# Performance work log

Measured on AMD Instinct MI355X. Metric: run time of the kernel, lower is better.

The kernel has to match this reference:

```python
import jax, jax.numpy as jnp
from jax import lax
import numpy as np

GWS = (2, 7, 7)          # grid_window_size
NUM_HEADS = 4
DIM = 256
HEAD_DIM = DIM // NUM_HEADS
SCALE = HEAD_DIM ** -0.5


def _rel_index(ws):
    d, h, w = ws
    coords = np.stack(np.meshgrid(np.arange(d), np.arange(h), np.arange(w), indexing='ij')).reshape(3, -1)
    rel = (coords[:, :, None] - coords[:, None, :]).transpose(1, 2, 0)
    rel[:, :, 0] += d - 1
    rel[:, :, 1] += h - 1
    rel[:, :, 2] += w - 1
    rel[:, :, 0] *= (2 * h - 1) * (2 * w - 1)
    rel[:, :, 1] *= (2 * w - 1)
    return rel.sum(-1)

RPI = jnp.asarray(_rel_index(GWS))  # (98, 98) int, constant buffer


def _ln(x, w, b, eps=1e-5):
    m = x.mean(-1, keepdims=True)
    v = ((x - m) ** 2).mean(-1, keepdims=True)
    return (x - m) * lax.rsqrt(v + eps) * w + b


def _attention(x, qkv_w, proj_w, proj_b, bias_table):
    # x: (num_windows, N, C); qkv has no bias in the original (qkv_bias=False)
    Bw, N, C = x.shape
    qkv = (x @ qkv_w.T).reshape(Bw, N, 3, NUM_HEADS, HEAD_DIM).transpose(2, 0, 3, 1, 4)
    q, k, v = qkv[0] * SCALE, qkv[1], qkv[2]
    scores = jnp.einsum('bhnd,bhmd->bhnm', q, k)
    bias = bias_table[RPI.reshape(-1)].reshape(N, N, NUM_HEADS).transpose(2, 0, 1)
    a = jax.nn.softmax(scores + bias[None], axis=-1)
    out = jnp.einsum('bhnm,bhmd->bhnd', a, v).transpose(0, 2, 1, 3).reshape(Bw, N, C)
    return out @ proj_w.T + proj_b


def _window_partition(x):
    B, D, H, W, C = x.shape
    d, h, w = GWS
    x = x.reshape(B, D // d, d, H // h, h, W // w, w, C).transpose(0, 1, 3, 5, 2, 4, 6, 7)
    return x.reshape(-1, d * h * w, C)


def _window_reverse(win, B, D, H, W):
    d, h, w = GWS
    x = win.reshape(B, D // d, H // h, W // w, d, h, w, -1).transpose(0, 1, 4, 2, 5, 3, 6, 7)
    return x.reshape(B, D, H, W, -1)


def _grid_partition(x):
    B, D, H, W, C = x.shape
    d, h, w = GWS
    x = x.reshape(B, d, D // d, h, H // h, w, W // w, C).transpose(0, 2, 4, 6, 1, 3, 5, 7)
    return x.reshape(-1, d * h * w, C)


def _grid_reverse(g, B, D, H, W):
    d, h, w = GWS
    x = g.reshape(B, D // d, H // h, W // w, d, h, w, -1).transpose(0, 4, 1, 5, 2, 6, 3, 7)
    return x.reshape(B, D, H, W, -1)


def _conv3d(x, w, b):
    y = lax.conv_general_dilated(x, w, (1, 1, 1), 'SAME',
                                 dimension_numbers=('NCDHW', 'OIDHW', 'NCDHW'))
    return y + b[None, :, None, None, None]


def _leaky(x):
    return jnp.where(x >= 0, x, 0.01 * x)


def setup_inputs() -> dict:
    key = jax.random.key(0)
    ks = jax.random.split(key, 12)
    B, D, H, W = 2, 8, 56, 56
    dim = DIM
    TBL = (2 * GWS[0] - 1) * (2 * GWS[1] - 1) * (2 * GWS[2] - 1)  # 507
    p = lambda k, s: jax.random.normal(k, s, jnp.float32) * 0.02
    return {
        'input': jax.random.normal(ks[0], (B, dim, D, H, W), jnp.float32),
        'n1w': jnp.ones((dim,), jnp.float32), 'n1b': jnp.zeros((dim,), jnp.float32),
        'n2w': jnp.ones((dim,), jnp.float32), 'n2b': jnp.zeros((dim,), jnp.float32),
        'wqkv': p(ks[1], (3 * dim, dim)),
        'wprojw': p(ks[2], (dim, dim)), 'wprojb': jnp.zeros((dim,), jnp.float32),
        'wbias': p(ks[3], (TBL, NUM_HEADS)),
        'gqkv': p(ks[4], (3 * dim, dim)),
        'gprojw': p(ks[5], (dim, dim)), 'gprojb': jnp.zeros((dim,), jnp.float32),
        'gbias': p(ks[6], (TBL, NUM_HEADS)),
        'f1c1w': p(ks[7], (128, 128, 3, 3, 3)), 'f1c1b': jnp.zeros((128,), jnp.float32),
        'f1c2w': p(ks[8], (128, 128, 3, 3, 3)), 'f1c2b': jnp.zeros((128,), jnp.float32),
        'g1c1w': p(ks[9], (128, 128, 3, 3, 3)), 'g1c1b': jnp.zeros((128,), jnp.float32),
        'g1c2w': p(ks[10], (128, 128, 3, 3, 3)), 'g1c2b': jnp.zeros((128,), jnp.float32),
    }


def reference(input, n1w, n1b, n2w, n2b, wqkv, wprojw, wprojb, wbias,
              gqkv, gprojw, gprojb, gbias,
              f1c1w, f1c1b, f1c2w, f1c2b, g1c1w, g1c1b, g1c2w, g1c2b):
    B, C, D, H, W = input.shape
    x = input.transpose(0, 2, 3, 4, 1)  # b d h w c
    x = _ln(x, n1w, n1b)
    pd = (GWS[0] - D % GWS[0]) % GWS[0]
    ph = (GWS[1] - H % GWS[1]) % GWS[1]
    pw = (GWS[2] - W % GWS[2]) % GWS[2]
    if pd or ph or pw:
        x = jnp.pad(x, ((0, 0), (0, pd), (0, ph), (0, pw), (0, 0)))
    Dp, Hp, Wp = D + pd, H + ph, W + pw
    # block (window) attention
    win = _window_partition(x)
    win = _attention(win, wqkv, wprojw, wprojb, wbias)
    xw = _window_reverse(win, B, Dp, Hp, Wp)
    # grid attention
    y = _ln(xw, n2w, n2b)
    g = _grid_partition(y)
    g = _attention(g, gqkv, gprojw, gprojb, gbias)
    y = _grid_reverse(g, B, Dp, Hp, Wp) + xw
    if pd or ph or pw:
        y = y[:, :D, :H, :W, :]
    y = y.transpose(0, 4, 1, 2, 3)  # b c d h w
    s = input + y
    # reversible conv block: split 256 -> 128/128
    x1, x2 = s[:, :C // 2], s[:, C // 2:]
    y1 = x1 + _conv3d(_leaky(_conv3d(x2, f1c1w, f1c1b)), f1c2w, f1c2b)
    y2 = x2 + _conv3d(_leaky(_conv3d(y1, g1c1w, g1c1b)), g1c2w, g1c2b)
    return jnp.concatenate([y1, y2], axis=1)
```

## Files before the change

### kernel.cpp

```cpp
#include <hip/hip_runtime.h>
#include <stdint.h>


typedef unsigned short u16;
typedef __attribute__((ext_vector_type(8))) short short8;
typedef __attribute__((ext_vector_type(4))) float f32x4;

#define TOK   50176
#define CH    256
#define SPAT  25088
#define PLANE 3136

__device__ __forceinline__ float b2f(u16 u) {
    union { uint32_t i; float f; } v; v.i = ((uint32_t)u) << 16; return v.f;
}
__device__ __forceinline__ u16 f2b(float f) {
    union { float f; uint32_t i; } v; v.f = f;
    uint32_t i = v.i;
    uint32_t r = i + 0x7FFFu + ((i >> 16) & 1u);
    return (u16)(r >> 16);
}

__global__ __launch_bounds__(256) void cvtw_kernel(
    const float* __restrict__ src, u16* __restrict__ dst)
{
    int i = (blockIdx.x * 256 + threadIdx.x) * 4;
    float4 v = *(const float4*)(src + i);
    ushort4 p;
    p.x = f2b(v.x); p.y = f2b(v.y); p.z = f2b(v.z); p.w = f2b(v.w);
    *(ushort4*)(dst + i) = p;
}

__global__ __launch_bounds__(256) void ln1_kernel(
    const float* __restrict__ x, const float* __restrict__ w,
    const float* __restrict__ bsh, u16* __restrict__ out)
{
    int t = blockIdx.x * 256 + threadIdx.x;
    int b = t / SPAT, sp = t % SPAT;
    const float* px = x + (size_t)b * CH * SPAT + sp;
    float s = 0.f, ss = 0.f;
    for (int c = 0; c < CH; c++) { float v = px[(size_t)c * SPAT]; s += v; ss += v * v; }
    float mean = s * (1.0f / CH);
    float var  = ss * (1.0f / CH) - mean * mean;
    float rstd = rsqrtf(var + 1e-5f);
    u16* po = out + (size_t)t * CH;
    for (int c = 0; c < CH; c++) {
        float v = (px[(size_t)c * SPAT] - mean) * rstd * w[c] + bsh[c];
        po[c] = f2b(v);
    }
}

__global__ __launch_bounds__(256) void ln2_kernel(
    const u16* __restrict__ x, const float* __restrict__ w,
    const float* __restrict__ bsh, u16* __restrict__ out)
{
    int wave = threadIdx.x >> 6, lane = threadIdx.x & 63;
    int t = blockIdx.x * 4 + wave;
    const u16* px = x + (size_t)t * CH + lane * 4;
    ushort4 v4 = *(const ushort4*)px;
    float v0 = b2f(v4.x), v1 = b2f(v4.y), v2 = b2f(v4.z), v3 = b2f(v4.w);
    float s = v0 + v1 + v2 + v3;
    float ss = v0*v0 + v1*v1 + v2*v2 + v3*v3;
    for (int o = 32; o > 0; o >>= 1) {
        s  += __shfl_xor(s,  o, 64);
        ss += __shfl_xor(ss, o, 64);
    }
    float mean = s * (1.0f / CH);
    float rstd = rsqrtf(ss * (1.0f / CH) - mean * mean + 1e-5f);
    float4 w4 = *(const float4*)(w + lane * 4);
    float4 b4 = *(const float4*)(bsh + lane * 4);
    ushort4 o4;
    o4.x = f2b((v0 - mean) * rstd * w4.x + b4.x);
    o4.y = f2b((v1 - mean) * rstd * w4.y + b4.y);
    o4.z = f2b((v2 - mean) * rstd * w4.z + b4.z);
    o4.w = f2b((v3 - mean) * rstd * w4.w + b4.w);
    *(ushort4*)(out + (size_t)t * CH + lane * 4) = o4;
}

__global__ __launch_bounds__(256) void gemm_mfma_kernel(
    const u16* __restrict__ A, const u16* __restrict__ B,
    const float* __restrict__ bias, const u16* __restrict__ res,
    u16* __restrict__ C, int Nout)
{
    __shared__ u16 sAg[128][72];
    __shared__ u16 sBg[128][72];
    int tid = threadIdx.x;
    int m0 = blockIdx.x * 128, n0g = blockIdx.y * 128;
    int lane = tid & 63, wv = tid >> 6;
    int quad = lane >> 4, l15 = lane & 15;
    int mw = (wv & 1) * 64, nw = (wv >> 1) * 64;

    f32x4 zz = {0.f, 0.f, 0.f, 0.f};
    f32x4 acc[4][4];
    #pragma unroll
    for (int i = 0; i < 4; i++)
        #pragma unroll
        for (int j = 0; j < 4; j++) acc[i][j] = zz;

    for (int kc = 0; kc < 256; kc += 64) {
        __syncthreads();
        #pragma unroll
        for (int i = 0; i < 4; i++) {
            int unit = tid + i * 256;
            int row = unit >> 3, k8 = (unit & 7) << 3;
            *(uint4*)&sAg[row][k8] = *(const uint4*)(A + (size_t)(m0 + row) * 256 + kc + k8);
        }
        #pragma unroll
        for (int i = 0; i < 4; i++) {
            int unit = tid + i * 256;
            int row = unit >> 3, k8 = (unit & 7) << 3;
            *(uint4*)&sBg[row][k8] = *(const uint4*)(B + (size_t)(n0g + row) * 256 + kc + k8);
        }
        __syncthreads();
        #pragma unroll
        for (int kk = 0; kk < 2; kk++) {
            short8 afr[4], bfr[4];
            #pragma unroll
            for (int mt = 0; mt < 4; mt++)
                afr[mt] = *(const short8*)&sAg[mw + mt*16 + l15][kk*32 + quad*8];
            #pragma unroll
            for (int nt = 0; nt < 4; nt++)
                bfr[nt] = *(const short8*)&sBg[nw + nt*16 + l15][kk*32 + quad*8];
            #pragma unroll
            for (int mt = 0; mt < 4; mt++)
                #pragma unroll
                for (int nt = 0; nt < 4; nt++)
                    acc[mt][nt] = __builtin_amdgcn_mfma_f32_16x16x32_bf16(
                        afr[mt], bfr[nt], acc[mt][nt], 0, 0, 0);
        }
    }

    #pragma unroll
    for (int nt = 0; nt < 4; nt++) {
        int n = n0g + nw + nt*16 + l15;
        float bv = bias ? bias[n] : 0.f;
        #pragma unroll
        for (int mt = 0; mt < 4; mt++) {
            int m = m0 + mw + mt*16 + quad*4;
            #pragma unroll
            for (int r = 0; r < 4; r++) {
                float v = acc[mt][nt][r] + bv;
                size_t off = (size_t)(m + r) * Nout + n;
                if (res) v += b2f(res[off]);
                C[off] = f2b(v);
            }
        }
    }
}

__global__ __launch_bounds__(256) void attn_mfma_kernel(
    const u16* __restrict__ qkv, const float* __restrict__ btab,
    u16* __restrict__ outp, int mode)
{
    __shared__ u16 sKV[8704];
    __shared__ u16 sS[112][136];
    __shared__ float sBias[507];
    __shared__ int sTok[112];
    __shared__ int sEnc[112];
    __shared__ float sInv[112];

    int g = blockIdx.x, head = blockIdx.y, tid = threadIdx.x;
    int b  = g >> 8;
    int gd = (g >> 6) & 3, gh = (g >> 3) & 7, gw = g & 7;

    int lane = tid & 63, wv = tid >> 6;
    int quad = lane >> 4, l15 = lane & 15;
    int mts[2] = {wv, wv + 4};

    if (tid < 112) {
        int t = tid;
        int i = t / 49, r = t % 49, j = r / 7, k = r % 7;
        sEnc[tid] = i * 169 + j * 13 + k;
        int tokv = 0;
        if (t < 98) {
            int d, h, w;
            if (mode == 0) { d = gd*2 + i; h = gh*7 + j; w = gw*7 + k; }
            else           { d = i*4 + gd; h = j*8 + gh; w = k*8 + gw; }
            tokv = ((b*8 + d)*56 + h)*56 + w;
        }
        sTok[tid] = tokv;
    }
    for (int idx = tid; idx < 507; idx += 256) sBias[idx] = btab[idx * 4 + head];
    __syncthreads();

    for (int idx = tid; idx < 112 * 8; idx += 256) {
        int row = idx >> 3, c8 = (idx & 7) << 3;
        uint4 v = {0u, 0u, 0u, 0u};
        if (row < 98)
            v = *(const uint4*)(qkv + (size_t)sTok[row] * 768 + 256 + head * 64 + c8);
        *(uint4*)&sKV[row * 72 + c8] = v;
    }
    __syncthreads();

    short8 qf[2][2];
    #pragma unroll
    for (int mi = 0; mi < 2; mi++) {
        int mt = mts[mi];
        #pragma unroll
        for (int ks = 0; ks < 2; ks++) {
            short8 v;
            #pragma unroll
            for (int j = 0; j < 8; j++) v[j] = 0;
            int row = mt * 16 + l15;
            if (mt < 7 && row < 98)
                v = *(const short8*)(qkv + (size_t)sTok[row] * 768 + head * 64 + ks * 32 + quad * 8);
            qf[mi][ks] = v;
        }
    }

    f32x4 zz = {0.f, 0.f, 0.f, 0.f};
    #pragma unroll
    for (int mi = 0; mi < 2; mi++) {
        int mt = mts[mi];
        if (mt >= 7) continue;
        for (int nt = 0; nt < 7; nt++) {
            f32x4 acc = zz;
            acc = __builtin_amdgcn_mfma_f32_16x16x32_bf16(
                qf[mi][0], *(const short8*)&sKV[(nt*16 + l15) * 72 + quad*8], acc, 0, 0, 0);
            acc = __builtin_amdgcn_mfma_f32_16x16x32_bf16(
                qf[mi][1], *(const short8*)&sKV[(nt*16 + l15) * 72 + 32 + quad*8], acc, 0, 0, 0);
            int n = nt * 16 + l15;
            int en = (n < 98) ? sEnc[n] : 0;
            #pragma unroll
            for (int r = 0; r < 4; r++) {
                int m = mt * 16 + quad * 4 + r;
                float v;
                if (n < 98) {
                    int em = sEnc[m < 98 ? m : 97];
                    v = acc[r] * 0.125f + sBias[em - en + 253];
                } else v = -1e30f;
                sS[m][n] = f2b(v);
            }
        }
    }
    __syncthreads();

    for (int idx = tid; idx < 64 * 30; idx += 256) {
        int c = idx / 30, t = 98 + idx % 30;
        sKV[c * 136 + t] = 0;
    }
    for (int idx = tid; idx < 98 * 8; idx += 256) {
        int tok = idx >> 3, c8 = (idx & 7) << 3;
        uint4 v = *(const uint4*)(qkv + (size_t)sTok[tok] * 768 + 512 + head * 64 + c8);
        const u16* pv = (const u16*)&v;
        #pragma unroll
        for (int j = 0; j < 8; j++) sKV[(c8 + j) * 136 + tok] = pv[j];
    }

    {
        int row = tid >> 1, half = tid & 1;
        if (row < 112) {
            #pragma unroll
            for (int j = 0; j < 8; j++) sS[row][112 + half * 8 + j] = 0;
        }
        if (row < 98) {
            int c0 = half * 49;
            float mx = -1e30f;
            for (int j = 0; j < 49; j++) mx = fmaxf(mx, b2f(sS[row][c0 + j]));
            mx = fmaxf(mx, __shfl_xor(mx, 1, 64));
            float sum = 0.f;
            for (int j = 0; j < 49; j++) {
                float e = __expf(b2f(sS[row][c0 + j]) - mx);
                sum += e;
                sS[row][c0 + j] = f2b(e);
            }
            sum += __shfl_xor(sum, 1, 64);
            if (half == 0) sInv[row] = 1.0f / sum;
        }
    }
    __syncthreads();

    f32x4 po[2][4];
    #pragma unroll
    for (int mi = 0; mi < 2; mi++)
        #pragma unroll
        for (int nt = 0; nt < 4; nt++) po[mi][nt] = zz;

    #pragma unroll
    for (int mi = 0; mi < 2; mi++) {
        int mt = mts[mi];
        if (mt >= 7) continue;
        for (int ks = 0; ks < 4; ks++) {
            short8 ap = *(const short8*)&sS[mt*16 + l15][ks*32 + quad*8];
            #pragma unroll
            for (int nt = 0; nt < 4; nt++) {
                short8 bv = *(const short8*)&sKV[(nt*16 + l15) * 136 + ks*32 + quad*8];
                po[mi][nt] = __builtin_amdgcn_mfma_f32_16x16x32_bf16(ap, bv, po[mi][nt], 0, 0, 0);
            }
        }
    }

    #pragma unroll
    for (int mi = 0; mi < 2; mi++) {
        int mt = mts[mi];
        if (mt >= 7) continue;
        #pragma unroll
        for (int r = 0; r < 4; r++) {
            int m = mt * 16 + quad * 4 + r;
            if (m >= 98) continue;
            float inv = sInv[m];
            u16* dst = outp + (size_t)sTok[m] * 256 + head * 64 + l15;
            #pragma unroll
            for (int nt = 0; nt < 4; nt++)
                dst[nt * 16] = f2b(po[mi][nt][r] * inv);
        }
    }
}

__global__ __launch_bounds__(256) void ssplit_cl_kernel(
    const float* __restrict__ inp, const u16* __restrict__ y,
    u16* __restrict__ s1, u16* __restrict__ s2)
{
    __shared__ float sT[64][65];
    int t0 = blockIdx.x * 64;
    int b = t0 / SPAT, sp0 = t0 % SPAT;
    int tid = threadIdx.x;
    for (int cg = 0; cg < 4; cg++) {
        __syncthreads();
        #pragma unroll
        for (int i = 0; i < 16; i++) {
            int unit = tid + i * 256;
            int cl = unit >> 6, spl = unit & 63;
            sT[spl][cl] = inp[((size_t)(b * 256 + cg * 64 + cl)) * SPAT + sp0 + spl];
        }
        __syncthreads();
        int spl = tid >> 2, c16 = (tid & 3) * 16;
        int tok = t0 + spl;
        const u16* yp = y + (size_t)tok * 256 + cg * 64 + c16;
        int cbase = cg * 64 + c16;
        u16* dst = (cbase < 128) ? (s1 + (size_t)tok * 128 + cbase)
                                 : (s2 + (size_t)tok * 128 + cbase - 128);
        #pragma unroll
        for (int j = 0; j < 16; j++) {
            float v = sT[spl][c16 + j] + b2f(yp[j]);
            dst[j] = f2b(v);
        }
    }
}

__global__ __launch_bounds__(256) void convw_kernel(
    const float* __restrict__ w, u16* __restrict__ o)
{
    int e = blockIdx.x * 256 + threadIdx.x;
    int tap = e >> 14;
    int r = e & 16383;
    int kk = r >> 12;
    int nt = (r >> 9) & 7;
    int quad = (r >> 7) & 3;
    int l15 = (r >> 3) & 15;
    int j = r & 7;
    int oc = nt * 16 + l15;
    int ic = kk * 32 + quad * 8 + j;
    o[e] = f2b(w[(size_t)(oc * 128 + ic) * 27 + tap]);
}

__global__ __launch_bounds__(256, 4) void conv_mfma_kernel(
    const u16* __restrict__ in_cl,
    const u16* __restrict__ wtf,
    const float* __restrict__ bias,
    const u16* __restrict__ res_cl,
    u16* __restrict__ out_cl,
    float* __restrict__ out_f32,
    int oc_base, int leaky)
{
    __shared__ u16 sA[2][8192];

    int tid = threadIdx.x;
    int t0 = blockIdx.x * 64;
    int b = t0 / SPAT, sp0 = t0 % SPAT;

    int lane = tid & 63, wv = tid >> 6;
    int quad = lane >> 4, l15 = lane & 15;
    int n0 = wv * 32;
    int nbase = wv * 2;

    int ms  = wv * 16 + l15;
    int sp  = sp0 + ms;
    int d_s = sp / PLANE; int rr_ = sp % PLANE;
    int h_s = rr_ / 56, w_s = rr_ % 56;
    int lin_s = t0 + ms;
    const int icb = quad * 8;

    f32x4 zz = {0.f, 0.f, 0.f, 0.f};
    f32x4 acc[4][2];
    #pragma unroll
    for (int i = 0; i < 4; i++) { acc[i][0] = zz; acc[i][1] = zz; }

    uint4 pre[4];

    #define STAGE_REGS(TAP)                                                    \
    {                                                                          \
        const int kd = (TAP) / 9 - 1, kh = ((TAP) / 3) % 3 - 1,                \
                  kw = (TAP) % 3 - 1;                                          \
        int dd = d_s + kd, hh = h_s + kh, ww = w_s + kw;                       \
        bool ok = ((unsigned)dd < 8u) & ((unsigned)hh < 56u) &                 \
                  ((unsigned)ww < 56u);                                        \
        const u16* src = in_cl +                                               \
            (size_t)(lin_s + kd * PLANE + kh * 56 + kw) * 128 + icb;           \
        _Pragma("unroll")                                                      \
        for (int i = 0; i < 4; i++) {                                          \
            uint4 v = {0u, 0u, 0u, 0u};                                        \
            if (ok) v = *(const uint4*)(src + i * 32);                         \
            pre[i] = v;                                                        \
        }                                                                      \
    }

    STAGE_REGS(0);
    #pragma unroll
    for (int i = 0; i < 4; i++) *(uint4*)&sA[0][(tid + i * 256) * 8] = pre[i];
    __syncthreads();

    for (int tap = 0; tap < 27; tap++) {
        int cur = tap & 1;
        if (tap < 26) STAGE_REGS(tap + 1);

        const u16* wb = wtf + tap * 16384;
        #pragma unroll
        for (int kk = 0; kk < 4; kk++) {
            short8 afr[4], bfr[2];
            #pragma unroll
            for (int mt = 0; mt < 4; mt++)
                afr[mt] = *(const short8*)&sA[cur][((kk*4 + mt)*64 + lane) * 8];
            #pragma unroll
            for (int nt = 0; nt < 2; nt++)
                bfr[nt] = *(const short8*)(wb + ((kk*8 + nbase + nt)*64 + lane) * 8);
            #pragma unroll
            for (int mt = 0; mt < 4; mt++)
                #pragma unroll
                for (int nt = 0; nt < 2; nt++)
                    acc[mt][nt] = __builtin_amdgcn_mfma_f32_16x16x32_bf16(
                        afr[mt], bfr[nt], acc[mt][nt], 0, 0, 0);
        }

        if (tap < 26) {
            #pragma unroll
            for (int i = 0; i < 4; i++)
                *(uint4*)&sA[cur ^ 1][(tid + i * 256) * 8] = pre[i];
        }
        __syncthreads();
    }
    #undef STAGE_REGS

    #pragma unroll
    for (int nt = 0; nt < 2; nt++) {
        int oc = n0 + nt*16 + l15;
        float bv = bias[oc];
        #pragma unroll
        for (int mt = 0; mt < 4; mt++) {
            int m = mt*16 + quad*4;
            #pragma unroll
            for (int r = 0; r < 4; r++) {
                float v = acc[mt][nt][r] + bv;
                if (leaky) v = (v >= 0.f) ? v : 0.01f * v;
                if (res_cl) v += b2f(res_cl[(size_t)(t0 + m + r) * 128 + oc]);
                acc[mt][nt][r] = v;
            }
        }
    }

    if (out_cl) {
        #pragma unroll
        for (int mt = 0; mt < 4; mt++) {
            int m = mt*16 + quad*4;
            #pragma unroll
            for (int nt = 0; nt < 2; nt++) {
                int oc = n0 + nt*16 + l15;
                #pragma unroll
                for (int r = 0; r < 4; r++)
                    out_cl[(size_t)(t0 + m + r) * 128 + oc] = f2b(acc[mt][nt][r]);
            }
        }
    }

    if (out_f32) {
        __syncthreads();
        float* sT = (float*)&sA[0][0];
        #pragma unroll
        for (int mt = 0; mt < 4; mt++) {
            int m = mt*16 + quad*4;
            #pragma unroll
            for (int nt = 0; nt < 2; nt++) {
                int oc = n0 + nt*16 + l15;
                #pragma unroll
                for (int r = 0; r < 4; r++)
                    sT[oc * 64 + ((m + r + oc) & 63)] = acc[mt][nt][r];
            }
        }
        __syncthreads();
        int oc = tid >> 1, half = tid & 1;
        size_t obase = ((size_t)b * 256 + oc_base + oc) * SPAT + sp0 + half * 32;
        const float* row = &sT[oc * 64];
        for (int j = 0; j < 32; j++) {
            int m = half * 32 + j;
            out_f32[obase + j] = row[(m + oc) & 63];
        }
    }
}

extern "C" void kernel_launch(void* const* d_in, const int* in_sizes, int n_in,
                              void* d_out, int out_size, void* d_ws, size_t ws_size,
                              hipStream_t stream)
{
    const float* input  = (const float*)d_in[0];
    const float* n1w    = (const float*)d_in[1];
    const float* n1b    = (const float*)d_in[2];
    const float* n2w    = (const float*)d_in[3];
    const float* n2b    = (const float*)d_in[4];
    const float* wqkv   = (const float*)d_in[5];
    const float* wprojw = (const float*)d_in[6];
    const float* wprojb = (const float*)d_in[7];
    const float* wbias  = (const float*)d_in[8];
    const float* gqkv   = (const float*)d_in[9];
    const float* gprojw = (const float*)d_in[10];
    const float* gprojb = (const float*)d_in[11];
    const float* gbias  = (const float*)d_in[12];
    const float* f1c1w  = (const float*)d_in[13];
    const float* f1c1b  = (const float*)d_in[14];
    const float* f1c2w  = (const float*)d_in[15];
    const float* f1c2b  = (const float*)d_in[16];
    const float* g1c1w  = (const float*)d_in[17];
    const float* g1c1b  = (const float*)d_in[18];
    const float* g1c2w  = (const float*)d_in[19];
    const float* g1c2b  = (const float*)d_in[20];

    char* ws = (char*)d_ws;
    u16* xln   = (u16*)(ws);
    u16* qkv   = (u16*)(ws + 25690112);
    u16* attnb = (u16*)(ws + 102760448);
    u16* xw    = (u16*)(ws + 128450560);
    u16* y  = xln;
    u16* s1   = qkv;
    u16* s2   = (u16*)(ws + 25690112 + 12845056);
    u16* tb   = (u16*)(ws + 25690112 + 25690112);
    u16* y1cl = (u16*)(ws + 25690112 + 38535168);
    u16* cw0  = (u16*)(ws + 25690112 + 51380224);
    u16* cw1  = cw0 + 442368;
    u16* cw2  = cw1 + 442368;
    u16* cw3  = cw2 + 442368;

    float* outp = (float*)d_out;

    u16* wqkvB  = (u16*)d_out;
    u16* gqkvB  = wqkvB + 196608;
    u16* wprojB = gqkvB + 196608;
    u16* gprojB = wprojB + 65536;

    cvtw_kernel<<<192, 256, 0, stream>>>(wqkv,   wqkvB);
    cvtw_kernel<<<192, 256, 0, stream>>>(gqkv,   gqkvB);
    cvtw_kernel<<<64,  256, 0, stream>>>(wprojw, wprojB);
    cvtw_kernel<<<64,  256, 0, stream>>>(gprojw, gprojB);
    ln1_kernel<<<196, 256, 0, stream>>>(input, n1w, n1b, xln);
    gemm_mfma_kernel<<<dim3(392, 6), 256, 0, stream>>>(xln, wqkvB, nullptr, nullptr, qkv, 768);
    attn_mfma_kernel<<<dim3(512, 4), 256, 0, stream>>>(qkv, wbias, attnb, 0);
    gemm_mfma_kernel<<<dim3(392, 2), 256, 0, stream>>>(attnb, wprojB, wprojb, nullptr, xw, 256);
    ln2_kernel<<<12544, 256, 0, stream>>>(xw, n2w, n2b, xln);
    gemm_mfma_kernel<<<dim3(392, 6), 256, 0, stream>>>(xln, gqkvB, nullptr, nullptr, qkv, 768);
    attn_mfma_kernel<<<dim3(512, 4), 256, 0, stream>>>(qkv, gbias, attnb, 1);
    gemm_mfma_kernel<<<dim3(392, 2), 256, 0, stream>>>(attnb, gprojB, gprojb, xw, y, 256);
    ssplit_cl_kernel<<<784, 256, 0, stream>>>(input, y, s1, s2);
    convw_kernel<<<1728, 256, 0, stream>>>(f1c1w, cw0);
    convw_kernel<<<1728, 256, 0, stream>>>(f1c2w, cw1);
    convw_kernel<<<1728, 256, 0, stream>>>(g1c1w, cw2);
    convw_kernel<<<1728, 256, 0, stream>>>(g1c2w, cw3);
    conv_mfma_kernel<<<784, 256, 0, stream>>>(s2, cw0, f1c1b, nullptr, tb, nullptr, 0, 1);
    conv_mfma_kernel<<<784, 256, 0, stream>>>(tb, cw1, f1c2b, s1, y1cl, outp, 0, 0);
    conv_mfma_kernel<<<784, 256, 0, stream>>>(y1cl, cw2, g1c1b, nullptr, tb, nullptr, 0, 1);
    conv_mfma_kernel<<<784, 256, 0, stream>>>(tb, cw3, g1c2b, s2, nullptr, outp, 128, 0);
}
```

Before: 833.9 us.

## Retile conv MFMA warps to 2x4 tiles and prefetch weight fragments

Each wave in the conv kernel used to compute 4 token tiles by 2 output-channel tiles. It now computes 2 token tiles by 4 output-channel tiles, so the four waves form a 2x2 grid over tokens and channels. Weight fragments are double-buffered in registers, so the next kk or tap's B loads are issued before the current MFMAs, hiding global weight-load latency. The occupancy hint is lowered from 4 to 3 blocks per CU to leave room for the extra registers, which risks less latency hiding across waves.

After: 988.9 us. 1.19x slower.

```diff
diff --git a/kernel.cpp b/kernel.cpp
--- a/kernel.cpp
+++ b/kernel.cpp
@@ -354,7 +354,7 @@
     o[e] = f2b(w[(size_t)(oc * 128 + ic) * 27 + tap]);
 }
 
-__global__ __launch_bounds__(256, 4) void conv_mfma_kernel(
+__global__ __launch_bounds__(256, 3) void conv_mfma_kernel(
     const u16* __restrict__ in_cl,
     const u16* __restrict__ wtf,
     const float* __restrict__ bias,
@@ -371,8 +371,8 @@
 
     int lane = tid & 63, wv = tid >> 6;
     int quad = lane >> 4, l15 = lane & 15;
-    int n0 = wv * 32;
-    int nbase = wv * 2;
+    int tokgrp = wv & 1, och = wv >> 1;
+    int ntb = och * 4;
 
     int ms  = wv * 16 + l15;
     int sp  = sp0 + ms;
@@ -382,9 +382,11 @@
     const int icb = quad * 8;
 
     f32x4 zz = {0.f, 0.f, 0.f, 0.f};
-    f32x4 acc[4][2];
-    #pragma unroll
-    for (int i = 0; i < 4; i++) { acc[i][0] = zz; acc[i][1] = zz; }
+    f32x4 acc[2][4];
+    #pragma unroll
+    for (int i = 0; i < 2; i++)
+        #pragma unroll
+        for (int j = 0; j < 4; j++) acc[i][j] = zz;
 
     uint4 pre[4];
 
@@ -405,31 +407,48 @@
         }                                                                      \
     }
 
+    #define LOADB(DST, TAP, KK)                                                \
+    {                                                                          \
+        const u16* wp_ = wtf + (size_t)(TAP) * 16384;                          \
+        _Pragma("unroll")                                                      \
+        for (int nt_ = 0; nt_ < 4; nt_++)                                      \
+            DST[nt_] = *(const short8*)(wp_ +                                  \
+                (((KK) * 8 + ntb + nt_) * 64 + lane) * 8);                     \
+    }
+
     STAGE_REGS(0);
     #pragma unroll
     for (int i = 0; i < 4; i++) *(uint4*)&sA[0][(tid + i * 256) * 8] = pre[i];
     __syncthreads();
+
+    short8 bcur[4], bnext[4];
+    LOADB(bcur, 0, 0);
 
     for (int tap = 0; tap < 27; tap++) {
         int cur = tap & 1;
         if (tap < 26) STAGE_REGS(tap + 1);
 
-        const u16* wb = wtf + tap * 16384;
         #pragma unroll
         for (int kk = 0; kk < 4; kk++) {
-            short8 afr[4], bfr[2];
-            #pragma unroll
-            for (int mt = 0; mt < 4; mt++)
-                afr[mt] = *(const short8*)&sA[cur][((kk*4 + mt)*64 + lane) * 8];
-            #pragma unroll
-            for (int nt = 0; nt < 2; nt++)
-                bfr[nt] = *(const short8*)(wb + ((kk*8 + nbase + nt)*64 + lane) * 8);
-            #pragma unroll
-            for (int mt = 0; mt < 4; mt++)
+            if (kk < 3) {
+                LOADB(bnext, tap, kk + 1);
+            } else if (tap < 26) {
+                LOADB(bnext, tap + 1, 0);
+            }
+            short8 afr[2];
+            #pragma unroll
+            for (int mi = 0; mi < 2; mi++) {
+                int mt = tokgrp * 2 + mi;
+                afr[mi] = *(const short8*)&sA[cur][((kk*4 + mt)*64 + lane) * 8];
+            }
+            #pragma unroll
+            for (int mi = 0; mi < 2; mi++)
                 #pragma unroll
-                for (int nt = 0; nt < 2; nt++)
-                    acc[mt][nt] = __builtin_amdgcn_mfma_f32_16x16x32_bf16(
-                        afr[mt], bfr[nt], acc[mt][nt], 0, 0, 0);
+                for (int nt = 0; nt < 4; nt++)
+                    acc[mi][nt] = __builtin_amdgcn_mfma_f32_16x16x32_bf16(
+                        afr[mi], bcur[nt], acc[mi][nt], 0, 0, 0);
+            #pragma unroll
+            for (int nt = 0; nt < 4; nt++) bcur[nt] = bnext[nt];
         }
 
         if (tap < 26) {
@@ -440,34 +459,35 @@
         __syncthreads();
     }
     #undef STAGE_REGS
-
-    #pragma unroll
-    for (int nt = 0; nt < 2; nt++) {
-        int oc = n0 + nt*16 + l15;
+    #undef LOADB
+
+    #pragma unroll
+    for (int nt = 0; nt < 4; nt++) {
+        int oc = och * 64 + nt*16 + l15;
         float bv = bias[oc];
         #pragma unroll
-        for (int mt = 0; mt < 4; mt++) {
-            int m = mt*16 + quad*4;
+        for (int mi = 0; mi < 2; mi++) {
+            int m = (tokgrp*2 + mi)*16 + quad*4;
             #pragma unroll
             for (int r = 0; r < 4; r++) {
-                float v = acc[mt][nt][r] + bv;
+                float v = acc[mi][nt][r] + bv;
                 if (leaky) v = (v >= 0.f) ? v : 0.01f * v;
                 if (res_cl) v += b2f(res_cl[(size_t)(t0 + m + r) * 128 + oc]);
-                acc[mt][nt][r] = v;
+                acc[mi][nt][r] = v;
             }
         }
     }
 
     if (out_cl) {
         #pragma unroll
-        for (int mt = 0; mt < 4; mt++) {
-            int m = mt*16 + quad*4;
-            #pragma unroll
-            for (int nt = 0; nt < 2; nt++) {
-                int oc = n0 + nt*16 + l15;
+        for (int mi = 0; mi < 2; mi++) {
+            int m = (tokgrp*2 + mi)*16 + quad*4;
+            #pragma unroll
+            for (int nt = 0; nt < 4; nt++) {
+                int oc = och * 64 + nt*16 + l15;
                 #pragma unroll
                 for (int r = 0; r < 4; r++)
-                    out_cl[(size_t)(t0 + m + r) * 128 + oc] = f2b(acc[mt][nt][r]);
+                    out_cl[(size_t)(t0 + m + r) * 128 + oc] = f2b(acc[mi][nt][r]);
             }
         }
     }
@@ -476,14 +496,14 @@
         __syncthreads();
         float* sT = (float*)&sA[0][0];
         #pragma unroll
-        for (int mt = 0; mt < 4; mt++) {
-            int m = mt*16 + quad*4;
-            #pragma unroll
-            for (int nt = 0; nt < 2; nt++) {
-                int oc = n0 + nt*16 + l15;
+        for (int mi = 0; mi < 2; mi++) {
+            int m = (tokgrp*2 + mi)*16 + quad*4;
+            #pragma unroll
+            for (int nt = 0; nt < 4; nt++) {
+                int oc = och * 64 + nt*16 + l15;
                 #pragma unroll
                 for (int r = 0; r < 4; r++)
-                    sT[oc * 64 + ((m + r + oc) & 63)] = acc[mt][nt][r];
+                    sT[oc * 64 + ((m + r + oc) & 63)] = acc[mi][nt][r];
             }
         }
         __syncthreads();
```
